# Optimization experiments

Hardware: AMD Instinct MI355X
Metric: run time of the kernel (lower is better)

## Reference

```python
import jax, jax.numpy as jnp
import numpy as np

N_NODES = 50000
N_EDGES = 800000
IN_CH = 128
OUT_CH = 64
HEADS = 2
NEG_SLOPE = 0.2


def _gat_conv(x, src, dst, W, a_src, a_dst, b, n):
    """PyG-style GATConv (eval mode: no dropout), self-loops already appended.
    x: [n, F_in]; W: [F_in, H*C]; a_src/a_dst: [H, C]; b: [H*C]."""
    H, C = a_src.shape
    h = (x @ W).reshape(n, H, C)                       # [n, H, C]
    alpha_src = jnp.sum(h * a_src, axis=-1)            # [n, H]
    alpha_dst = jnp.sum(h * a_dst, axis=-1)            # [n, H]
    e = alpha_src[src] + alpha_dst[dst]                # [E, H]
    e = jnp.where(e > 0, e, NEG_SLOPE * e)             # LeakyReLU(0.2)
    # neighbor-wise (destination-grouped) softmax, numerically stable
    m = jax.ops.segment_max(e, dst, num_segments=n)
    e = jnp.exp(e - m[dst])
    denom = jax.ops.segment_sum(e, dst, num_segments=n)
    alpha = e / (denom[dst] + 1e-16)                   # [E, H]
    out = jax.ops.segment_sum(alpha[:, :, None] * h[src], dst, num_segments=n)
    return out.reshape(n, H * C) + b


def setup_inputs() -> dict:
    key = jax.random.key(0)
    ks = jax.random.split(key, 12)
    s = 0.08  # glorot-ish scale
    x = jax.random.normal(ks[0], (N_NODES, IN_CH), dtype=jnp.float32)
    edge_index = jax.random.randint(ks[1], (2, N_EDGES), 0, N_NODES, dtype=jnp.int64)
    H, O = HEADS, OUT_CH
    return {
        "x": x,
        "edge_index": edge_index,
        "W1": jax.random.normal(ks[2], (IN_CH, H * 2 * O), dtype=jnp.float32) * s,
        "a_src1": jax.random.normal(ks[3], (H, 2 * O), dtype=jnp.float32) * s,
        "a_dst1": jax.random.normal(ks[4], (H, 2 * O), dtype=jnp.float32) * s,
        "b1": jnp.zeros((H * 2 * O,), dtype=jnp.float32),
        "W_mu": jax.random.normal(ks[5], (2 * O * H, H * O), dtype=jnp.float32) * s,
        "a_src_mu": jax.random.normal(ks[6], (H, O), dtype=jnp.float32) * s,
        "a_dst_mu": jax.random.normal(ks[7], (H, O), dtype=jnp.float32) * s,
        "b_mu": jnp.zeros((H * O,), dtype=jnp.float32),
        "W_ls": jax.random.normal(ks[8], (2 * O * H, H * O), dtype=jnp.float32) * s,
        "a_src_ls": jax.random.normal(ks[9], (H, O), dtype=jnp.float32) * s,
        "a_dst_ls": jax.random.normal(ks[10], (H, O), dtype=jnp.float32) * s,
        "b_ls": jnp.zeros((H * O,), dtype=jnp.float32),
    }


def reference(x, edge_index, W1, a_src1, a_dst1, b1,
              W_mu, a_src_mu, a_dst_mu, b_mu,
              W_ls, a_src_ls, a_dst_ls, b_ls):
    n = x.shape[0]
    loop = jnp.arange(n, dtype=edge_index.dtype)
    src = jnp.concatenate([edge_index[0], loop])  # PyG add_self_loops=True
    dst = jnp.concatenate([edge_index[1], loop])
    x1 = jax.nn.elu(_gat_conv(x, src, dst, W1, a_src1, a_dst1, b1, n))
    mu = _gat_conv(x1, src, dst, W_mu, a_src_mu, a_dst_mu, b_mu, n)
    logstd = _gat_conv(x1, src, dst, W_ls, a_src_ls, a_dst_ls, b_ls, n)
    return (mu, logstd)
```

## Files before the change

kernel.cpp:

```cpp
#include <hip/hip_runtime.h>


typedef unsigned short u16;
typedef unsigned int u32;
typedef _Float16 f16;
typedef f16 f16x8 __attribute__((ext_vector_type(8)));
typedef float f32x4v __attribute__((ext_vector_type(4)));

__device__ __forceinline__ u16 f2h(float f) {
    union { f16 h; u16 u; } t;
    t.h = (f16)f;
    return t.u;
}
__device__ __forceinline__ float4 loadh4(const u16* __restrict__ p, size_t i) {
    union { uint2 u; f16 h[4]; } t;
    t.u = *(const uint2*)(p + i);
    return make_float4((float)t.h[0], (float)t.h[1], (float)t.h[2], (float)t.h[3]);
}
__device__ __forceinline__ void store4(float* __restrict__ p, size_t i, float4 v) {
    *(float4*)(p + i) = v;
}
__device__ __forceinline__ void store4(u16* __restrict__ p, size_t i, float4 v) {
    union { uint2 u; f16 h[4]; } t;
    t.h[0] = (f16)v.x; t.h[1] = (f16)v.y; t.h[2] = (f16)v.z; t.h[3] = (f16)v.w;
    *(uint2*)(p + i) = t.u;
}

__global__ __launch_bounds__(256) void k_extract(const u32* __restrict__ ebuf, int E,
                                                 int* __restrict__ se,
                                                 int* __restrict__ de,
                                                 int* __restrict__ deg) {
    __shared__ int nz;
    if (threadIdx.x == 0) nz = 0;
    __syncthreads();
    if (ebuf[2 * threadIdx.x + 1] != 0u) atomicAdd(&nz, 1);
    __syncthreads();
    const bool i64 = (nz == 0);
    int e = blockIdx.x * 256 + threadIdx.x;
    if (e >= E) return;
    int s, d;
    if (i64) {
        s = (int)ebuf[2 * (size_t)e];
        d = (int)ebuf[2 * ((size_t)E + (size_t)e)];
    } else {
        s = (int)ebuf[e];
        d = (int)ebuf[(size_t)E + (size_t)e];
    }
    se[e] = s;
    de[e] = d;
    atomicAdd(&deg[d], 1);
}

__global__ __launch_bounds__(256) void k_scan_a(const int* __restrict__ deg, int n,
                                                int* __restrict__ bsum) {
    __shared__ int s[256];
    int i = blockIdx.x * 256 + threadIdx.x;
    s[threadIdx.x] = (i < n) ? deg[i] : 0;
    __syncthreads();
    for (int st = 128; st > 0; st >>= 1) {
        if (threadIdx.x < st) s[threadIdx.x] += s[threadIdx.x + st];
        __syncthreads();
    }
    if (threadIdx.x == 0) bsum[blockIdx.x] = s[0];
}

__global__ __launch_bounds__(256) void k_scan_b(int* __restrict__ bsum, int nb) {
    __shared__ int s[256];
    int t = threadIdx.x;
    int v = (t < nb) ? bsum[t] : 0;
    s[t] = v;
    __syncthreads();
    for (int off = 1; off < 256; off <<= 1) {
        int add = (t >= off) ? s[t - off] : 0;
        __syncthreads();
        s[t] += add;
        __syncthreads();
    }
    if (t < nb) bsum[t] = s[t] - v;
}

__global__ __launch_bounds__(256) void k_scan_c(const int* __restrict__ deg, int n,
                                                const int* __restrict__ bsum,
                                                int* __restrict__ rowptr,
                                                int* __restrict__ cursor, int E) {
    __shared__ int s[256];
    int t = threadIdx.x;
    int i = blockIdx.x * 256 + t;
    int v = (i < n) ? deg[i] : 0;
    s[t] = v;
    __syncthreads();
    for (int off = 1; off < 256; off <<= 1) {
        int add = (t >= off) ? s[t - off] : 0;
        __syncthreads();
        s[t] += add;
        __syncthreads();
    }
    if (i < n) {
        int ex = bsum[blockIdx.x] + s[t] - v;
        rowptr[i] = ex;
        cursor[i] = ex;
    }
    if (i == 0) rowptr[n] = E;
}

__global__ __launch_bounds__(256) void k_fill(const int* __restrict__ src,
                                              const int* __restrict__ dst, int E,
                                              int* __restrict__ cursor,
                                              int* __restrict__ csr_src,
                                              int* __restrict__ csr_dst) {
    int e = blockIdx.x * 256 + threadIdx.x;
    if (e < 8) csr_src[E + e] = 0;
    if (e < E) {
        int d = dst[e];
        int slot = atomicAdd(&cursor[d], 1);
        csr_src[slot] = src[e];
        csr_dst[slot] = d;
    }
}

__global__ __launch_bounds__(256) void k_tw(const float* __restrict__ Wl,
                                            const float* __restrict__ Wr, int split,
                                            int K, u16* __restrict__ Wt) {
    int idx = blockIdx.x * 256 + threadIdx.x;
    if (idx >= 256 * K) return;
    int c = idx / K, k = idx - c * K;
    float v;
    if (split == 256)
        v = Wl[(size_t)k * 256 + c];
    else
        v = (c < 128) ? Wl[(size_t)k * 128 + c] : Wr[(size_t)k * 128 + (c - 128)];
    Wt[idx] = f2h(v);
}

template <int NS>
__global__ __launch_bounds__(256) void k_w(const int* __restrict__ csr_src,
                                           const int* __restrict__ csr_dst,
                                           const float* __restrict__ as,
                                           const float* __restrict__ ad,
                                           float* __restrict__ wp, int E, int Ep) {
    int i = blockIdx.x * 256 + threadIdx.x;
    if (i >= E) return;
    int s = csr_src[i], d = csr_dst[i];
    if (NS == 2) {
        float2 a = *(const float2*)(as + (size_t)s * 2);
        float2 b = *(const float2*)(ad + (size_t)d * 2);
        float e0 = a.x + b.x, e1 = a.y + b.y;
        e0 = fmaxf(e0, 0.2f * e0);
        e1 = fmaxf(e1, 0.2f * e1);
        wp[i] = __expf(e0);
        wp[(size_t)Ep + i] = __expf(e1);
    } else {
        float4 a = *(const float4*)(as + (size_t)s * 4);
        float4 b = *(const float4*)(ad + (size_t)d * 4);
        float e0 = a.x + b.x, e1 = a.y + b.y, e2 = a.z + b.z, e3 = a.w + b.w;
        e0 = fmaxf(e0, 0.2f * e0);
        e1 = fmaxf(e1, 0.2f * e1);
        e2 = fmaxf(e2, 0.2f * e2);
        e3 = fmaxf(e3, 0.2f * e3);
        wp[i] = __expf(e0);
        wp[(size_t)Ep + i] = __expf(e1);
        wp[2 * (size_t)Ep + i] = __expf(e2);
        wp[3 * (size_t)Ep + i] = __expf(e3);
    }
}

template <int K, int ALOGW, bool AF32>
__global__ __launch_bounds__(256) void k_gemm_mfma(
    const void* __restrict__ Av, const u16* __restrict__ Wt, u16* __restrict__ out,
    float* __restrict__ as_out, float* __restrict__ ad_out,
    const float* __restrict__ alo, const float* __restrict__ ahi,
    const float* __restrict__ dlo, const float* __restrict__ dhi, int M) {
    __shared__ u16 Bs[256 * 40];
    const int tid = threadIdx.x;
    const int wave = tid >> 6;
    const int lane = tid & 63;
    const int li = lane & 15;
    const int quad = lane >> 4;
    const int r0 = blockIdx.x * 128 + wave * 32;
    int ar0 = r0 + li;
    int ar1 = r0 + 16 + li;
    if (ar0 >= M) ar0 = M - 1;
    if (ar1 >= M) ar1 = M - 1;
    const u16* a16_0 = (const u16*)Av + (size_t)ar0 * K + quad * 8;
    const u16* a16_1 = (const u16*)Av + (size_t)ar1 * K + quad * 8;
    const float* a32_0 = (const float*)Av + (size_t)ar0 * K + quad * 8;
    const float* a32_1 = (const float*)Av + (size_t)ar1 * K + quad * 8;

    f32x4v acc0[16], acc1[16];
#pragma unroll
    for (int ct = 0; ct < 16; ct++) {
        acc0[ct] = (f32x4v)(0.f);
        acc1[ct] = (f32x4v)(0.f);
    }

    const u16* wrow = Wt + (size_t)tid * K;
    u16* dstp = Bs + tid * 40;
    uint4 sv0 = ((const uint4*)wrow)[0];
    uint4 sv1 = ((const uint4*)(wrow + 8))[0];
    uint4 sv2 = ((const uint4*)(wrow + 16))[0];
    uint4 sv3 = ((const uint4*)(wrow + 24))[0];
    uint4 p0a, p0b, p1a, p1b;
    if (AF32) {
        p0a = *(const uint4*)(a32_0);
        p0b = *(const uint4*)(a32_0 + 4);
        p1a = *(const uint4*)(a32_1);
        p1b = *(const uint4*)(a32_1 + 4);
    } else {
        p0a = *(const uint4*)(a16_0);
        p1a = *(const uint4*)(a16_1);
        p0b = p0a;
        p1b = p1a;
    }

    for (int t = 0; t < K; t += 32) {
        asm volatile("s_waitcnt lgkmcnt(0)" ::: "memory");
        __builtin_amdgcn_s_barrier();
        ((uint4*)dstp)[0] = sv0;
        ((uint4*)(dstp + 8))[0] = sv1;
        ((uint4*)(dstp + 16))[0] = sv2;
        ((uint4*)(dstp + 24))[0] = sv3;
        f16x8 a0, a1;
        if (AF32) {
            union { uint4 u; float f[4]; } ua, ub;
            ua.u = p0a; ub.u = p0b;
            a0[0] = (f16)ua.f[0]; a0[1] = (f16)ua.f[1];
            a0[2] = (f16)ua.f[2]; a0[3] = (f16)ua.f[3];
            a0[4] = (f16)ub.f[0]; a0[5] = (f16)ub.f[1];
            a0[6] = (f16)ub.f[2]; a0[7] = (f16)ub.f[3];
            ua.u = p1a; ub.u = p1b;
            a1[0] = (f16)ua.f[0]; a1[1] = (f16)ua.f[1];
            a1[2] = (f16)ua.f[2]; a1[3] = (f16)ua.f[3];
            a1[4] = (f16)ub.f[0]; a1[5] = (f16)ub.f[1];
            a1[6] = (f16)ub.f[2]; a1[7] = (f16)ub.f[3];
        } else {
            union { uint4 u; f16x8 h; } uh;
            uh.u = p0a; a0 = uh.h;
            uh.u = p1a; a1 = uh.h;
        }
        if (t + 32 < K) {
            const u16* s2 = wrow + t + 32;
            sv0 = ((const uint4*)s2)[0];
            sv1 = ((const uint4*)(s2 + 8))[0];
            sv2 = ((const uint4*)(s2 + 16))[0];
            sv3 = ((const uint4*)(s2 + 24))[0];
            if (AF32) {
                p0a = *(const uint4*)(a32_0 + t + 32);
                p0b = *(const uint4*)(a32_0 + t + 36);
                p1a = *(const uint4*)(a32_1 + t + 32);
                p1b = *(const uint4*)(a32_1 + t + 36);
            } else {
                p0a = *(const uint4*)(a16_0 + t + 32);
                p1a = *(const uint4*)(a16_1 + t + 32);
            }
        }
        asm volatile("s_waitcnt lgkmcnt(0)" ::: "memory");
        __builtin_amdgcn_s_barrier();
#pragma unroll
        for (int ct = 0; ct < 16; ct++) {
            f16x8 b = *(const f16x8*)(Bs + (ct * 16 + li) * 40 + quad * 8);
            acc0[ct] = __builtin_amdgcn_mfma_f32_16x16x32_f16(a0, b, acc0[ct], 0, 0, 0);
            acc1[ct] = __builtin_amdgcn_mfma_f32_16x16x32_f16(a1, b, acc1[ct], 0, 0, 0);
        }
    }

    const int NS = 64 >> ALOGW;
    const int SH = ALOGW - 2;
    float aw[16], dw[16];
#pragma unroll
    for (int ct = 0; ct < 16; ct++) {
        int col = ct * 16 + li;
        aw[ct] = (col < 128) ? alo[col] : ahi[col - 128];
        dw[ct] = (col < 128) ? dlo[col] : dhi[col - 128];
    }

    auto epilogue = [&](f32x4v(&acc)[16], int rbase) {
#pragma unroll
        for (int reg = 0; reg < 4; reg++) {
            int grow = rbase + quad * 4 + reg;
            if (grow < M) {
                u16* orow = out + (size_t)grow * 256 + li;
#pragma unroll
                for (int ct = 0; ct < 16; ct++) orow[ct * 16] = f2h(acc[ct][reg]);
            }
        }
#pragma unroll
        for (int reg = 0; reg < 4; reg++) {
            float s[4] = {0.f, 0.f, 0.f, 0.f};
            float d[4] = {0.f, 0.f, 0.f, 0.f};
#pragma unroll
            for (int ct = 0; ct < 16; ct++) {
                int sl = ct >> SH;
                s[sl] += acc[ct][reg] * aw[ct];
                d[sl] += acc[ct][reg] * dw[ct];
            }
#pragma unroll
            for (int sl = 0; sl < NS; sl++) {
#pragma unroll
                for (int m = 1; m <= 8; m <<= 1) {
                    s[sl] += __shfl_xor(s[sl], m, 64);
                    d[sl] += __shfl_xor(d[sl], m, 64);
                }
            }
            int grow = rbase + quad * 4 + reg;
            if (li == 0 && grow < M) {
#pragma unroll
                for (int sl = 0; sl < NS; sl++) {
                    as_out[(size_t)grow * NS + sl] = s[sl];
                    ad_out[(size_t)grow * NS + sl] = d[sl];
                }
            }
        }
    };
    epilogue(acc0, r0);
    epilogue(acc1, r0 + 16);
}

template <int LOGW, int MODE, typename OT>
__global__ __launch_bounds__(256) void k_agg5(
    const u16* __restrict__ h, const int* __restrict__ rowptr,
    const int* __restrict__ csr_src, const float* __restrict__ wp,
    const float* __restrict__ as, const float* __restrict__ ad,
    const float* __restrict__ b_lo, const float* __restrict__ b_hi,
    OT* __restrict__ outp, int n, int nGrp, int Ep) {
    const int NS = 64 >> LOGW;
    const int bid = blockIdx.x;
    const int xcd = bid & 7;
    const int half = xcd >> 2;
    const int grp = (bid >> 3) * 4 + (xcd & 3);
    if (grp >= nGrp) return;
    const int lane = threadIdx.x & 63;
    const int sub = lane >> 5;
    const int sl = lane & 31;
    const int wid0 = grp * 8 + (threadIdx.x >> 6) * 2 + sub;
    const bool ok = wid0 < n;
    const int wid = ok ? wid0 : (n - 1);
    const int col = half * 128 + sl * 4;
    const int slot = col >> (LOGW + 2);
    const float* __restrict__ wpl = wp + (size_t)slot * Ep;

    float e = as[(size_t)wid * NS + slot] + ad[(size_t)wid * NS + slot];
    e = fmaxf(e, 0.2f * e);
    float w = __expf(e);
    float denom = w;
    float4 hv = loadh4(h, (size_t)wid * 256 + col);
    float acc0 = w * hv.x, acc1 = w * hv.y, acc2 = w * hv.z, acc3 = w * hv.w;

    int rb = 0, re = 0;
    if (ok) { rb = rowptr[wid0]; re = rowptr[wid0 + 1]; }
    for (int p = rb; p < re; p += 8) {
        int4 sA = *(const int4*)(csr_src + p);
        int4 sB = *(const int4*)(csr_src + p + 4);
        float4 wA = *(const float4*)(wpl + p);
        float4 wB = *(const float4*)(wpl + p + 4);
        int rem = re - p;
        float w0 = wA.x;
        float w1 = (rem > 1) ? wA.y : 0.f;
        float w2 = (rem > 2) ? wA.z : 0.f;
        float w3 = (rem > 3) ? wA.w : 0.f;
        float w4 = (rem > 4) ? wB.x : 0.f;
        float w5 = (rem > 5) ? wB.y : 0.f;
        float w6 = (rem > 6) ? wB.z : 0.f;
        float w7 = (rem > 7) ? wB.w : 0.f;
        float4 h0 = loadh4(h, (size_t)sA.x * 256 + col);
        float4 h1 = loadh4(h, (size_t)sA.y * 256 + col);
        float4 h2 = loadh4(h, (size_t)sA.z * 256 + col);
        float4 h3 = loadh4(h, (size_t)sA.w * 256 + col);
        float4 h4 = loadh4(h, (size_t)sB.x * 256 + col);
        float4 h5 = loadh4(h, (size_t)sB.y * 256 + col);
        float4 h6 = loadh4(h, (size_t)sB.z * 256 + col);
        float4 h7 = loadh4(h, (size_t)sB.w * 256 + col);
        denom += (w0 + w1 + w2 + w3) + (w4 + w5 + w6 + w7);
        acc0 += w0 * h0.x + w1 * h1.x + w2 * h2.x + w3 * h3.x +
                w4 * h4.x + w5 * h5.x + w6 * h6.x + w7 * h7.x;
        acc1 += w0 * h0.y + w1 * h1.y + w2 * h2.y + w3 * h3.y +
                w4 * h4.y + w5 * h5.y + w6 * h6.y + w7 * h7.y;
        acc2 += w0 * h0.z + w1 * h1.z + w2 * h2.z + w3 * h3.z +
                w4 * h4.z + w5 * h5.z + w6 * h6.z + w7 * h7.z;
        acc3 += w0 * h0.w + w1 * h1.w + w2 * h2.w + w3 * h3.w +
                w4 * h4.w + w5 * h5.w + w6 * h6.w + w7 * h7.w;
    }
    float inv = 1.0f / (denom + 1e-16f);

    const float* bp = half ? b_hi : b_lo;
    const int ci = sl * 4;
    float4 bv = *(const float4*)(bp + ci);
    float v0 = acc0 * inv + bv.x;
    float v1 = acc1 * inv + bv.y;
    float v2 = acc2 * inv + bv.z;
    float v3 = acc3 * inv + bv.w;

    if (!ok) return;
    if (MODE == 0) {
        v0 = v0 > 0.f ? v0 : expm1f(v0);
        v1 = v1 > 0.f ? v1 : expm1f(v1);
        v2 = v2 > 0.f ? v2 : expm1f(v2);
        v3 = v3 > 0.f ? v3 : expm1f(v3);
        store4((u16*)outp, (size_t)wid0 * 256 + col, make_float4(v0, v1, v2, v3));
    } else {
        size_t base = half ? ((size_t)n * 128 + (size_t)wid0 * 128 + ci)
                           : ((size_t)wid0 * 128 + ci);
        store4((float*)outp, base, make_float4(v0, v1, v2, v3));
    }
}

extern "C" void kernel_launch(void* const* d_in, const int* in_sizes, int n_in,
                              void* d_out, int out_size, void* d_ws, size_t ws_size,
                              hipStream_t stream) {
    const float* x = (const float*)d_in[0];
    const u32* ebuf = (const u32*)d_in[1];
    const float* W1 = (const float*)d_in[2];
    const float* a_src1 = (const float*)d_in[3];
    const float* a_dst1 = (const float*)d_in[4];
    const float* b1 = (const float*)d_in[5];
    const float* W_mu = (const float*)d_in[6];
    const float* a_src_mu = (const float*)d_in[7];
    const float* a_dst_mu = (const float*)d_in[8];
    const float* b_mu = (const float*)d_in[9];
    const float* W_ls = (const float*)d_in[10];
    const float* a_src_ls = (const float*)d_in[11];
    const float* a_dst_ls = (const float*)d_in[12];
    const float* b_ls = (const float*)d_in[13];

    const int n = in_sizes[0] / 128;
    const int E = in_sizes[1] / 2;
    const int Ep = E + 8;

    char* base = (char*)d_ws;
    size_t off = 0;
    auto alloc = [&](size_t b) -> char* {
        char* p = base + off;
        off = (off + b + 255) & ~(size_t)255;
        return p;
    };
    int* rowptr = (int*)alloc((size_t)(n + 1) * 4);
    int* cursor = (int*)alloc((size_t)n * 4);
    int* csr = (int*)alloc((size_t)Ep * 4);
    int* csrd = (int*)alloc((size_t)E * 4);
    int* bsum = (int*)alloc(256 * 4);
    int* se = (int*)alloc((size_t)E * 4);
    int* de = (int*)alloc((size_t)E * 4);
    float* as = (float*)alloc((size_t)n * 4 * 4);
    float* ad = (float*)alloc((size_t)n * 4 * 4);
    float* wp = (float*)alloc((size_t)Ep * 4 * 4);
    u16* W1t = (u16*)alloc(256 * 128 * 2);
    u16* Wt2 = (u16*)alloc(256 * 256 * 2);
    u16* x1h = (u16*)alloc((size_t)n * 256 * 2);
    u16* h = (u16*)alloc((size_t)n * 256 * 2);

    const int nb = (n + 255) / 256;
    const int eg = (E + 255) / 256;
    const int gg = (n + 127) / 128;
    const int nGrp = (n + 7) / 8;
    const int aggGrid = 8 * ((nGrp + 3) / 4);

    hipMemsetAsync(cursor, 0, (size_t)n * 4, stream);
    k_extract<<<eg, 256, 0, stream>>>(ebuf, E, se, de, cursor);
    k_scan_a<<<nb, 256, 0, stream>>>(cursor, n, bsum);
    k_scan_b<<<1, 256, 0, stream>>>(bsum, nb);
    k_scan_c<<<nb, 256, 0, stream>>>(cursor, n, bsum, rowptr, cursor, E);
    k_fill<<<eg, 256, 0, stream>>>(se, de, E, cursor, csr, csrd);

    k_tw<<<(256 * 128 + 255) / 256, 256, 0, stream>>>(W1, W1, 256, 128, W1t);
    k_tw<<<(256 * 256 + 255) / 256, 256, 0, stream>>>(W_mu, W_ls, 128, 256, Wt2);

    k_gemm_mfma<128, 5, true><<<gg, 256, 0, stream>>>(x, W1t, h, as, ad, a_src1,
                                                      a_src1 + 128, a_dst1,
                                                      a_dst1 + 128, n);
    k_w<2><<<eg, 256, 0, stream>>>(csr, csrd, as, ad, wp, E, Ep);
    k_agg5<5, 0, u16><<<aggGrid, 256, 0, stream>>>(h, rowptr, csr, wp, as, ad, b1,
                                                   b1 + 128, x1h, n, nGrp, Ep);

    k_gemm_mfma<256, 4, false><<<gg, 256, 0, stream>>>(x1h, Wt2, h, as, ad,
                                                       a_src_mu, a_src_ls,
                                                       a_dst_mu, a_dst_ls, n);
    k_w<4><<<eg, 256, 0, stream>>>(csr, csrd, as, ad, wp, E, Ep);
    k_agg5<4, 1, float><<<aggGrid, 256, 0, stream>>>(h, rowptr, csr, wp, as, ad,
                                                     b_mu, b_ls, (float*)d_out, n,
                                                     nGrp, Ep);
}
```

Before: 386.2 us.

## Aggregate full 256-column rows per half-wave with 16-byte gathers, dropping XCD column split

The aggregation kernel now has each 32-lane half-wave cover all 256 feature columns of a node, 8 fp16 values per lane via 16-byte loads. Before, the work was split into two column halves across blocks placed on separate XCD groups. This halves the grid, so per-node CSR indices and weights are read once instead of twice, and the gathers get wider. The 8-wide loop no longer masks out-of-range weights: it runs only on full chunks, with 4-wide and scalar tail loops after it. Costs are higher register pressure per thread and the loss of the XCD-aware L2 partitioning of the h columns.

```diff
diff --git a/kernel.cpp b/kernel.cpp
--- a/kernel.cpp
+++ b/kernel.cpp
@@ -12,18 +12,15 @@
     t.h = (f16)f;
     return t.u;
 }
-__device__ __forceinline__ float4 loadh4(const u16* __restrict__ p, size_t i) {
-    union { uint2 u; f16 h[4]; } t;
-    t.u = *(const uint2*)(p + i);
-    return make_float4((float)t.h[0], (float)t.h[1], (float)t.h[2], (float)t.h[3]);
+__device__ __forceinline__ void loadh8(const u16* __restrict__ p, size_t i,
+                                       float* __restrict__ o) {
+    union { uint4 u; f16 h[8]; } t;
+    t.u = *(const uint4*)(p + i);
+#pragma unroll
+    for (int j = 0; j < 8; j++) o[j] = (float)t.h[j];
 }
 __device__ __forceinline__ void store4(float* __restrict__ p, size_t i, float4 v) {
     *(float4*)(p + i) = v;
-}
-__device__ __forceinline__ void store4(u16* __restrict__ p, size_t i, float4 v) {
-    union { uint2 u; f16 h[4]; } t;
-    t.h[0] = (f16)v.x; t.h[1] = (f16)v.y; t.h[2] = (f16)v.z; t.h[3] = (f16)v.w;
-    *(uint2*)(p + i) = t.u;
 }
 
 __global__ __launch_bounds__(256) void k_extract(const u32* __restrict__ ebuf, int E,
@@ -316,25 +313,20 @@
 }
 
 template <int LOGW, int MODE, typename OT>
-__global__ __launch_bounds__(256) void k_agg5(
+__global__ __launch_bounds__(256) void k_agg6(
     const u16* __restrict__ h, const int* __restrict__ rowptr,
     const int* __restrict__ csr_src, const float* __restrict__ wp,
     const float* __restrict__ as, const float* __restrict__ ad,
     const float* __restrict__ b_lo, const float* __restrict__ b_hi,
-    OT* __restrict__ outp, int n, int nGrp, int Ep) {
+    OT* __restrict__ outp, int n, int Ep) {
     const int NS = 64 >> LOGW;
-    const int bid = blockIdx.x;
-    const int xcd = bid & 7;
-    const int half = xcd >> 2;
-    const int grp = (bid >> 3) * 4 + (xcd & 3);
-    if (grp >= nGrp) return;
     const int lane = threadIdx.x & 63;
     const int sub = lane >> 5;
     const int sl = lane & 31;
-    const int wid0 = grp * 8 + (threadIdx.x >> 6) * 2 + sub;
+    const int wid0 = blockIdx.x * 8 + (threadIdx.x >> 6) * 2 + sub;
     const bool ok = wid0 < n;
     const int wid = ok ? wid0 : (n - 1);
-    const int col = half * 128 + sl * 4;
+    const int col = sl * 8;
     const int slot = col >> (LOGW + 2);
     const float* __restrict__ wpl = wp + (size_t)slot * Ep;
 
@@ -342,64 +334,79 @@
     e = fmaxf(e, 0.2f * e);
     float w = __expf(e);
     float denom = w;
-    float4 hv = loadh4(h, (size_t)wid * 256 + col);
-    float acc0 = w * hv.x, acc1 = w * hv.y, acc2 = w * hv.z, acc3 = w * hv.w;
+    float acc[8], hb[8];
+    loadh8(h, (size_t)wid * 256 + col, hb);
+#pragma unroll
+    for (int c = 0; c < 8; c++) acc[c] = w * hb[c];
 
     int rb = 0, re = 0;
     if (ok) { rb = rowptr[wid0]; re = rowptr[wid0 + 1]; }
-    for (int p = rb; p < re; p += 8) {
+    int p = rb;
+    for (; p + 8 <= re; p += 8) {
         int4 sA = *(const int4*)(csr_src + p);
         int4 sB = *(const int4*)(csr_src + p + 4);
         float4 wA = *(const float4*)(wpl + p);
         float4 wB = *(const float4*)(wpl + p + 4);
-        int rem = re - p;
-        float w0 = wA.x;
-        float w1 = (rem > 1) ? wA.y : 0.f;
-        float w2 = (rem > 2) ? wA.z : 0.f;
-        float w3 = (rem > 3) ? wA.w : 0.f;
-        float w4 = (rem > 4) ? wB.x : 0.f;
-        float w5 = (rem > 5) ? wB.y : 0.f;
-        float w6 = (rem > 6) ? wB.z : 0.f;
-        float w7 = (rem > 7) ? wB.w : 0.f;
-        float4 h0 = loadh4(h, (size_t)sA.x * 256 + col);
-        float4 h1 = loadh4(h, (size_t)sA.y * 256 + col);
-        float4 h2 = loadh4(h, (size_t)sA.z * 256 + col);
-        float4 h3 = loadh4(h, (size_t)sA.w * 256 + col);
-        float4 h4 = loadh4(h, (size_t)sB.x * 256 + col);
-        float4 h5 = loadh4(h, (size_t)sB.y * 256 + col);
-        float4 h6 = loadh4(h, (size_t)sB.z * 256 + col);
-        float4 h7 = loadh4(h, (size_t)sB.w * 256 + col);
-        denom += (w0 + w1 + w2 + w3) + (w4 + w5 + w6 + w7);
-        acc0 += w0 * h0.x + w1 * h1.x + w2 * h2.x + w3 * h3.x +
-                w4 * h4.x + w5 * h5.x + w6 * h6.x + w7 * h7.x;
-        acc1 += w0 * h0.y + w1 * h1.y + w2 * h2.y + w3 * h3.y +
-                w4 * h4.y + w5 * h5.y + w6 * h6.y + w7 * h7.y;
-        acc2 += w0 * h0.z + w1 * h1.z + w2 * h2.z + w3 * h3.z +
-                w4 * h4.z + w5 * h5.z + w6 * h6.z + w7 * h7.z;
-        acc3 += w0 * h0.w + w1 * h1.w + w2 * h2.w + w3 * h3.w +
-                w4 * h4.w + w5 * h5.w + w6 * h6.w + w7 * h7.w;
+        float h0[8], h1[8], h2[8], h3[8], h4[8], h5[8], h6[8], h7[8];
+        loadh8(h, (size_t)sA.x * 256 + col, h0);
+        loadh8(h, (size_t)sA.y * 256 + col, h1);
+        loadh8(h, (size_t)sA.z * 256 + col, h2);
+        loadh8(h, (size_t)sA.w * 256 + col, h3);
+        loadh8(h, (size_t)sB.x * 256 + col, h4);
+        loadh8(h, (size_t)sB.y * 256 + col, h5);
+        loadh8(h, (size_t)sB.z * 256 + col, h6);
+        loadh8(h, (size_t)sB.w * 256 + col, h7);
+        denom += (wA.x + wA.y + wA.z + wA.w) + (wB.x + wB.y + wB.z + wB.w);
+#pragma unroll
+        for (int c = 0; c < 8; c++) {
+            acc[c] += wA.x * h0[c] + wA.y * h1[c] + wA.z * h2[c] + wA.w * h3[c] +
+                      wB.x * h4[c] + wB.y * h5[c] + wB.z * h6[c] + wB.w * h7[c];
+        }
+    }
+    for (; p + 4 <= re; p += 4) {
+        int4 sA = *(const int4*)(csr_src + p);
+        float4 wA = *(const float4*)(wpl + p);
+        float h0[8], h1[8], h2[8], h3[8];
+        loadh8(h, (size_t)sA.x * 256 + col, h0);
+        loadh8(h, (size_t)sA.y * 256 + col, h1);
+        loadh8(h, (size_t)sA.z * 256 + col, h2);
+        loadh8(h, (size_t)sA.w * 256 + col, h3);
+        denom += (wA.x + wA.y) + (wA.z + wA.w);
+#pragma unroll
+        for (int c = 0; c < 8; c++) {
+            acc[c] += wA.x * h0[c] + wA.y * h1[c] + wA.z * h2[c] + wA.w * h3[c];
+        }
+    }
+    for (; p < re; ++p) {
+        int s = csr_src[p];
+        float ww = wpl[p];
+        float hh[8];
+        loadh8(h, (size_t)s * 256 + col, hh);
+        denom += ww;
+#pragma unroll
+        for (int c = 0; c < 8; c++) acc[c] += ww * hh[c];
     }
     float inv = 1.0f / (denom + 1e-16f);
 
-    const float* bp = half ? b_hi : b_lo;
-    const int ci = sl * 4;
-    float4 bv = *(const float4*)(bp + ci);
-    float v0 = acc0 * inv + bv.x;
-    float v1 = acc1 * inv + bv.y;
-    float v2 = acc2 * inv + bv.z;
-    float v3 = acc3 * inv + bv.w;
+    const float* bp = (sl < 16) ? (b_lo + col) : (b_hi + (col - 128));
+    float v[8];
+#pragma unroll
+    for (int c = 0; c < 8; c++) v[c] = acc[c] * inv + bp[c];
 
     if (!ok) return;
     if (MODE == 0) {
-        v0 = v0 > 0.f ? v0 : expm1f(v0);
-        v1 = v1 > 0.f ? v1 : expm1f(v1);
-        v2 = v2 > 0.f ? v2 : expm1f(v2);
-        v3 = v3 > 0.f ? v3 : expm1f(v3);
-        store4((u16*)outp, (size_t)wid0 * 256 + col, make_float4(v0, v1, v2, v3));
+        union { uint4 u; f16 h[8]; } t;
+#pragma unroll
+        for (int c = 0; c < 8; c++) {
+            float vv = v[c] > 0.f ? v[c] : expm1f(v[c]);
+            t.h[c] = (f16)vv;
+        }
+        *(uint4*)((u16*)outp + (size_t)wid0 * 256 + col) = t.u;
     } else {
-        size_t base = half ? ((size_t)n * 128 + (size_t)wid0 * 128 + ci)
-                           : ((size_t)wid0 * 128 + ci);
-        store4((float*)outp, base, make_float4(v0, v1, v2, v3));
+        size_t base = (sl < 16) ? ((size_t)wid0 * 128 + col)
+                                : ((size_t)n * 128 + (size_t)wid0 * 128 + (col - 128));
+        store4((float*)outp, base, make_float4(v[0], v[1], v[2], v[3]));
+        store4((float*)outp, base + 4, make_float4(v[4], v[5], v[6], v[7]));
     }
 }
 
@@ -450,8 +457,7 @@
     const int nb = (n + 255) / 256;
     const int eg = (E + 255) / 256;
     const int gg = (n + 127) / 128;
-    const int nGrp = (n + 7) / 8;
-    const int aggGrid = 8 * ((nGrp + 3) / 4);
+    const int aggGrid = (n + 7) / 8;
 
     hipMemsetAsync(cursor, 0, (size_t)n * 4, stream);
     k_extract<<<eg, 256, 0, stream>>>(ebuf, E, se, de, cursor);
@@ -467,14 +473,14 @@
                                                       a_src1 + 128, a_dst1,
                                                       a_dst1 + 128, n);
     k_w<2><<<eg, 256, 0, stream>>>(csr, csrd, as, ad, wp, E, Ep);
-    k_agg5<5, 0, u16><<<aggGrid, 256, 0, stream>>>(h, rowptr, csr, wp, as, ad, b1,
-                                                   b1 + 128, x1h, n, nGrp, Ep);
+    k_agg6<5, 0, u16><<<aggGrid, 256, 0, stream>>>(h, rowptr, csr, wp, as, ad, b1,
+                                                   b1 + 128, x1h, n, Ep);
 
     k_gemm_mfma<256, 4, false><<<gg, 256, 0, stream>>>(x1h, Wt2, h, as, ad,
                                                        a_src_mu, a_src_ls,
                                                        a_dst_mu, a_dst_ls, n);
     k_w<4><<<eg, 256, 0, stream>>>(csr, csrd, as, ad, wp, E, Ep);
-    k_agg5<4, 1, float><<<aggGrid, 256, 0, stream>>>(h, rowptr, csr, wp, as, ad,
+    k_agg6<4, 1, float><<<aggGrid, 256, 0, stream>>>(h, rowptr, csr, wp, as, ad,
                                                      b_mu, b_ls, (float*)d_out, n,
-                                                     nGrp, Ep);
-}
+                                                     Ep);
+}
```

Measured after the change: 396.6 us. +2.7%, slower.
